# Performance work log

Measured on AMD Instinct MI355X. Metric: run time of the kernel, lower is better.

Reference implementation:

```python
import jax, jax.numpy as jnp
from jax import lax
import numpy as np

K = 8          # kernels per group
G = 64         # groups
_G = G // 2    # groups per diff branch (divisor=2 since g>1)
NUM_DIL = 7    # int(log2((1024-1)/8)) + 1


def _normalize(W):
    # match HydraInternal.normalize: zero-mean over taps, L1-normalize over taps
    W = W - W.mean(-1, keepdims=True)
    return W / jnp.abs(W).sum(-1, keepdims=True)


def setup_inputs() -> dict:
    key = jax.random.key(0)
    kx, kw = jax.random.split(key)
    X = jax.random.normal(kx, (256, 1, 1024), dtype=jnp.float32)
    # one (divisor=2, k*_g=256, in=1, taps=9) filter bank per dilation, stacked
    W = jax.random.normal(kw, (NUM_DIL, 2, K * _G, 1, 9), dtype=jnp.float32)
    W = _normalize(W)
    return {"X": X, "W": W}


def reference(X, W):
    N = X.shape[0]
    diff_X = jnp.diff(X, axis=-1)  # (N, 1, L-1)
    n_idx = jnp.arange(N)[:, None, None]
    g_idx = jnp.arange(_G)[None, :, None]
    feats = []
    for di in range(NUM_DIL):
        d = 2 ** di
        p = (8 * d) // 2
        for diff_index in range(2):
            inp = X if diff_index == 0 else diff_X
            # conv1d, dilation d, symmetric padding p -> (N, k*_g, Lz)
            Z = lax.conv_general_dilated(
                inp, W[di, diff_index], window_strides=(1,),
                padding=[(p, p)], rhs_dilation=(d,),
                dimension_numbers=("NCH", "OIH", "NCH"))
            Lz = Z.shape[-1]
            Zr = Z.reshape(N, _G, K, Lz)
            max_v = Zr.max(axis=2)          # (N, _g, Lz)
            max_i = Zr.argmax(axis=2)       # which of the k kernels won
            min_i = Zr.argmin(axis=2)
            count_max = jnp.zeros((N, _G, K), Zr.dtype).at[n_idx, g_idx, max_i].add(max_v)
            count_min = jnp.zeros((N, _G, K), Zr.dtype).at[n_idx, g_idx, min_i].add(1.0)
            feats.append(count_max)
            feats.append(count_min)
    return jnp.concatenate(feats, axis=1).reshape(N, -1)  # (N, 7168)
```

## Files before the change

kernel.cpp:

```cpp
#include <hip/hip_runtime.h>

#define NPAD 256
#define LDSX 1536

__device__ __forceinline__ float to_sgpr(float v) {
  return __int_as_float(__builtin_amdgcn_readfirstlane(__float_as_int(v)));
}

__device__ __forceinline__ float wredf(float x) {
  x += __int_as_float(__builtin_amdgcn_update_dpp(0, __float_as_int(x), 0x111, 0xf, 0xf, true));
  x += __int_as_float(__builtin_amdgcn_update_dpp(0, __float_as_int(x), 0x112, 0xf, 0xf, true));
  x += __int_as_float(__builtin_amdgcn_update_dpp(0, __float_as_int(x), 0x114, 0xf, 0xf, true));
  x += __int_as_float(__builtin_amdgcn_update_dpp(0, __float_as_int(x), 0x118, 0xf, 0xf, true));
  x += __int_as_float(__builtin_amdgcn_update_dpp(0, __float_as_int(x), 0x142, 0xa, 0xf, true));
  x += __int_as_float(__builtin_amdgcn_update_dpp(0, __float_as_int(x), 0x143, 0xc, 0xf, true));
  return x;
}
__device__ __forceinline__ int wredi(int x) {
  x += __builtin_amdgcn_update_dpp(0, x, 0x111, 0xf, 0xf, true);
  x += __builtin_amdgcn_update_dpp(0, x, 0x112, 0xf, 0xf, true);
  x += __builtin_amdgcn_update_dpp(0, x, 0x114, 0xf, 0xf, true);
  x += __builtin_amdgcn_update_dpp(0, x, 0x118, 0xf, 0xf, true);
  x += __builtin_amdgcn_update_dpp(0, x, 0x142, 0xa, 0xf, true);
  x += __builtin_amdgcn_update_dpp(0, x, 0x143, 0xc, 0xf, true);
  return x;
}

__global__ void __launch_bounds__(256, 3) hydra_kernel(
    const float* __restrict__ X, const float* __restrict__ W,
    float* __restrict__ out) {
  __shared__ float xs[LDSX];

  const int b = blockIdx.x;
  const int n = b / 14;
  const int r = b - n * 14;
  const int diff = r & 1;
  const int d = 1 << (r >> 1);
  const int Lz = 1024 - diff;
  const float* xrow = X + n * 1024;
  const int tid = threadIdx.x;
  const float qnan = __int_as_float(0x7fc00000);

  for (int i = tid; i < LDSX; i += 256) {
    int t = i - NPAD;
    float v = 0.0f;
    if (t >= 0 && t < Lz) v = diff ? (xrow[t + 1] - xrow[t]) : xrow[t];
    xs[i] = v;
  }
  __syncthreads();

  const int lane = tid & 63;
  const int wv = tid >> 6;
  const float* wb = W + r * 2304;
  float* outb = out + (size_t)n * 7168 + r * 512;

  for (int gp = 0; gp < 8; ++gp) {
    const int g = wv * 8 + gp;

    float w[72];
    {
      const float4* w4 = (const float4*)(wb + g * 72);
      #pragma unroll
      for (int q = 0; q < 18; ++q) {
        float4 v = w4[q];
        w[q * 4 + 0] = to_sgpr(v.x); w[q * 4 + 1] = to_sgpr(v.y);
        w[q * 4 + 2] = to_sgpr(v.z); w[q * 4 + 3] = to_sgpr(v.w);
      }
    }

    float cmax[8];
    int cmin[8];
    #pragma unroll
    for (int k = 0; k < 8; ++k) { cmax[k] = 0.0f; cmin[k] = 0; }

    const int base0 = NPAD - 4 * d + lane;

    #pragma unroll 4
    for (int it = 0; it < 16; ++it) {
      const int t = it * 64 + lane;

      float xv[9];
      #pragma unroll
      for (int j = 0; j < 9; ++j) xv[j] = xs[base0 + it * 64 + j * d];

      float z[8];
      #pragma unroll
      for (int k = 0; k < 8; ++k) {
        float a = w[k * 9] * xv[0];
        #pragma unroll
        for (int j = 1; j < 9; ++j) a = fmaf(w[k * 9 + j], xv[j], a);
        z[k] = a;
      }

      const float mA = fmaxf(fmaxf(z[0], z[1]), z[2]);
      const float mB = fmaxf(fmaxf(z[3], z[4]), z[5]);
      const float mC = fmaxf(z[6], z[7]);
      const float mx = fmaxf(fmaxf(mA, mB), mC);
      const float iA = fminf(fminf(z[0], z[1]), z[2]);
      const float iB = fminf(fminf(z[3], z[4]), z[5]);
      const float iC = fminf(z[6], z[7]);
      const float mn = fminf(fminf(iA, iB), iC);
      const float mn_eff = (t < Lz) ? mn : qnan;

      #pragma unroll
      for (int k = 0; k < 8; ++k) {
        cmax[k] += (z[k] == mx) ? z[k] : 0.0f;
        cmin[k] += (z[k] == mn_eff) ? 1 : 0;
      }
    }

    #pragma unroll
    for (int k = 0; k < 8; ++k) cmax[k] = wredf(cmax[k]);
    int cminr[8];
    #pragma unroll
    for (int k = 0; k < 8; ++k) cminr[k] = wredi(cmin[k]);

    if (lane == 63) {
      float4 a0 = make_float4(cmax[0], cmax[1], cmax[2], cmax[3]);
      float4 a1 = make_float4(cmax[4], cmax[5], cmax[6], cmax[7]);
      float4 b0 = make_float4((float)cminr[0], (float)cminr[1],
                              (float)cminr[2], (float)cminr[3]);
      float4 b1 = make_float4((float)cminr[4], (float)cminr[5],
                              (float)cminr[6], (float)cminr[7]);
      float4* pm = (float4*)(outb + g * 8);
      pm[0] = a0; pm[1] = a1;
      float4* pn = (float4*)(outb + 256 + g * 8);
      pn[0] = b0; pn[1] = b1;
    }
  }
}

extern "C" void kernel_launch(void* const* d_in, const int* in_sizes, int n_in,
                              void* d_out, int out_size, void* d_ws, size_t ws_size,
                              hipStream_t stream) {
  const float* X = (const float*)d_in[0];
  const float* W = (const float*)d_in[1];
  float* out = (float*)d_out;
  hydra_kernel<<<dim3(256 * 14), dim3(256), 0, stream>>>(X, W, out);
}
```

Baseline: 318.9 us.

## Split groups across 4x more blocks, templatize dilation, peel tail iteration

Launches four times as many blocks, each handling two groups per wave instead of eight, to raise parallelism and occupancy. Dilation becomes a template parameter so LDS offsets are compile-time immediates. The last iteration is peeled so the validity mask only applies to the tail, and min-counting uses an inline-asm compare plus add-with-carry. The cost is that each block now reloads and recomputes the shared input row, four times the total LDS fill work.

Result: faster. 307.0 us (-3.7%).

```diff
diff --git a/kernel.cpp b/kernel.cpp
--- a/kernel.cpp
+++ b/kernel.cpp
@@ -5,6 +5,12 @@
 
 __device__ __forceinline__ float to_sgpr(float v) {
   return __int_as_float(__builtin_amdgcn_readfirstlane(__float_as_int(v)));
+}
+
+__device__ __forceinline__ void cnt_eq(int& c, float z, float m) {
+  asm("v_cmp_eq_f32 vcc, %1, %2\n\t"
+      "v_addc_co_u32 %0, vcc, 0, %0, vcc"
+      : "+v"(c) : "v"(z), "v"(m) : "vcc");
 }
 
 __device__ __forceinline__ float wredf(float x) {
@@ -26,36 +32,15 @@
   return x;
 }
 
-__global__ void __launch_bounds__(256, 3) hydra_kernel(
-    const float* __restrict__ X, const float* __restrict__ W,
-    float* __restrict__ out) {
-  __shared__ float xs[LDSX];
-
-  const int b = blockIdx.x;
-  const int n = b / 14;
-  const int r = b - n * 14;
-  const int diff = r & 1;
-  const int d = 1 << (r >> 1);
+template <int D>
+__device__ __forceinline__ void conv_body(
+    const float* __restrict__ xs, int diff, int lane, int wv, int gh,
+    const float* __restrict__ wb, float* __restrict__ outb) {
   const int Lz = 1024 - diff;
-  const float* xrow = X + n * 1024;
-  const int tid = threadIdx.x;
   const float qnan = __int_as_float(0x7fc00000);
 
-  for (int i = tid; i < LDSX; i += 256) {
-    int t = i - NPAD;
-    float v = 0.0f;
-    if (t >= 0 && t < Lz) v = diff ? (xrow[t + 1] - xrow[t]) : xrow[t];
-    xs[i] = v;
-  }
-  __syncthreads();
-
-  const int lane = tid & 63;
-  const int wv = tid >> 6;
-  const float* wb = W + r * 2304;
-  float* outb = out + (size_t)n * 7168 + r * 512;
-
-  for (int gp = 0; gp < 8; ++gp) {
-    const int g = wv * 8 + gp;
+  for (int gp = 0; gp < 2; ++gp) {
+    const int g = gh * 8 + wv * 2 + gp;
 
     float w[72];
     {
@@ -73,15 +58,13 @@
     #pragma unroll
     for (int k = 0; k < 8; ++k) { cmax[k] = 0.0f; cmin[k] = 0; }
 
-    const int base0 = NPAD - 4 * d + lane;
+    const float* xp = xs + (NPAD - 4 * D) + lane;
 
-    #pragma unroll 4
-    for (int it = 0; it < 16; ++it) {
-      const int t = it * 64 + lane;
-
+    #pragma unroll 3
+    for (int it = 0; it < 15; ++it) {
       float xv[9];
       #pragma unroll
-      for (int j = 0; j < 9; ++j) xv[j] = xs[base0 + it * 64 + j * d];
+      for (int j = 0; j < 9; ++j) xv[j] = xp[it * 64 + j * D];
 
       float z[8];
       #pragma unroll
@@ -92,20 +75,45 @@
         z[k] = a;
       }
 
-      const float mA = fmaxf(fmaxf(z[0], z[1]), z[2]);
-      const float mB = fmaxf(fmaxf(z[3], z[4]), z[5]);
-      const float mC = fmaxf(z[6], z[7]);
-      const float mx = fmaxf(fmaxf(mA, mB), mC);
-      const float iA = fminf(fminf(z[0], z[1]), z[2]);
-      const float iB = fminf(fminf(z[3], z[4]), z[5]);
-      const float iC = fminf(z[6], z[7]);
-      const float mn = fminf(fminf(iA, iB), iC);
-      const float mn_eff = (t < Lz) ? mn : qnan;
-
+      const float mx = fmaxf(fmaxf(fmaxf(fmaxf(z[0], z[1]), z[2]),
+                                   fmaxf(fmaxf(z[3], z[4]), z[5])),
+                             fmaxf(z[6], z[7]));
+      const float mn = fminf(fminf(fminf(fminf(z[0], z[1]), z[2]),
+                                   fminf(fminf(z[3], z[4]), z[5])),
+                             fminf(z[6], z[7]));
       #pragma unroll
       for (int k = 0; k < 8; ++k) {
         cmax[k] += (z[k] == mx) ? z[k] : 0.0f;
-        cmin[k] += (z[k] == mn_eff) ? 1 : 0;
+        cnt_eq(cmin[k], z[k], mn);
+      }
+    }
+
+    {
+      float xv[9];
+      #pragma unroll
+      for (int j = 0; j < 9; ++j) xv[j] = xp[15 * 64 + j * D];
+
+      float z[8];
+      #pragma unroll
+      for (int k = 0; k < 8; ++k) {
+        float a = w[k * 9] * xv[0];
+        #pragma unroll
+        for (int j = 1; j < 9; ++j) a = fmaf(w[k * 9 + j], xv[j], a);
+        z[k] = a;
+      }
+      const float mx = fmaxf(fmaxf(fmaxf(fmaxf(z[0], z[1]), z[2]),
+                                   fmaxf(fmaxf(z[3], z[4]), z[5])),
+                             fmaxf(z[6], z[7]));
+      const float mn = fminf(fminf(fminf(fminf(z[0], z[1]), z[2]),
+                                   fminf(fminf(z[3], z[4]), z[5])),
+                             fminf(z[6], z[7]));
+      const bool valid = (960 + lane) < Lz;
+      const float mx_eff = valid ? mx : qnan;
+      const float mn_eff = valid ? mn : qnan;
+      #pragma unroll
+      for (int k = 0; k < 8; ++k) {
+        cmax[k] += (z[k] == mx_eff) ? z[k] : 0.0f;
+        cnt_eq(cmin[k], z[k], mn_eff);
       }
     }
 
@@ -130,11 +138,51 @@
   }
 }
 
+__global__ void __launch_bounds__(256, 3) hydra_kernel(
+    const float* __restrict__ X, const float* __restrict__ W,
+    float* __restrict__ out) {
+  __shared__ float xs[LDSX];
+
+  const int b = blockIdx.x;
+  const int gh = b & 3;
+  const int t1 = b >> 2;
+  const int r = t1 % 14;
+  const int n = t1 / 14;
+  const int diff = r & 1;
+  const int di = r >> 1;
+  const int Lz = 1024 - diff;
+  const float* xrow = X + n * 1024;
+  const int tid = threadIdx.x;
+
+  for (int i = tid; i < LDSX; i += 256) {
+    int t = i - NPAD;
+    float v = 0.0f;
+    if (t >= 0 && t < Lz) v = diff ? (xrow[t + 1] - xrow[t]) : xrow[t];
+    xs[i] = v;
+  }
+  __syncthreads();
+
+  const int lane = tid & 63;
+  const int wv = tid >> 6;
+  const float* wb = W + r * 2304;
+  float* outb = out + (size_t)n * 7168 + r * 512;
+
+  switch (di) {
+    case 0: conv_body<1 >(xs, diff, lane, wv, gh, wb, outb); break;
+    case 1: conv_body<2 >(xs, diff, lane, wv, gh, wb, outb); break;
+    case 2: conv_body<4 >(xs, diff, lane, wv, gh, wb, outb); break;
+    case 3: conv_body<8 >(xs, diff, lane, wv, gh, wb, outb); break;
+    case 4: conv_body<16>(xs, diff, lane, wv, gh, wb, outb); break;
+    case 5: conv_body<32>(xs, diff, lane, wv, gh, wb, outb); break;
+    default: conv_body<64>(xs, diff, lane, wv, gh, wb, outb); break;
+  }
+}
+
 extern "C" void kernel_launch(void* const* d_in, const int* in_sizes, int n_in,
                               void* d_out, int out_size, void* d_ws, size_t ws_size,
                               hipStream_t stream) {
   const float* X = (const float*)d_in[0];
   const float* W = (const float*)d_in[1];
   float* out = (float*)d_out;
-  hydra_kernel<<<dim3(256 * 14), dim3(256), 0, stream>>>(X, W, out);
+  hydra_kernel<<<dim3(256 * 14 * 4), dim3(256), 0, stream>>>(X, W, out);
 }
```
